# Kernel tuning notes

Hardware: AMD Instinct MI355X
Metric: run time of the kernel (lower is better)

## Reference

```python
import jax, jax.numpy as jnp
import numpy as np

N_NODES = 50000
N_EDGES = 1600000
DIM_IN = 128
DIM_OUT = 128
EPS = 1e-10


def setup_inputs() -> dict:
    key = jax.random.key(0)
    k1, k2, k3, k4, k5 = jax.random.split(key, 5)
    feat_in = jax.random.normal(k1, (N_NODES, DIM_IN), dtype=jnp.float32)
    rows = jax.random.randint(k2, (N_EDGES,), 0, N_NODES, dtype=jnp.int32)
    cols = jax.random.randint(k3, (N_EDGES,), 0, N_NODES, dtype=jnp.int32)
    # normalized adjacency values (positive, ~1/deg scale)
    vals = jax.random.uniform(k4, (N_EDGES,), dtype=jnp.float32) / 32.0
    W = jax.random.normal(k5, (DIM_OUT, DIM_IN), dtype=jnp.float32) * 0.05
    b = jnp.zeros((DIM_OUT,), dtype=jnp.float32)
    scale = jnp.ones((DIM_OUT,), dtype=jnp.float32)
    offset = jnp.zeros((DIM_OUT,), dtype=jnp.float32)
    return {"feat_in": feat_in, "rows": rows, "cols": cols, "vals": vals,
            "W": W, "b": b, "scale": scale, "offset": offset}


def reference(feat_in, rows, cols, vals, W, b, scale, offset):
    # torch.sparse.mm(adj_norm, feat_in): gather source features, scale by
    # edge value, scatter-add into destination rows.
    msgs = vals[:, None] * feat_in[cols]                       # [E, D_in]
    feat_aggr = jax.ops.segment_sum(msgs, rows, num_segments=N_NODES)  # [N, D_in]
    # f_lin (nn.Linear): x @ W.T + b
    feat_trans = feat_aggr @ W.T + b                           # [N, D_out]
    # act = ReLU
    a = jax.nn.relu(feat_trans)
    # f_norm: per-row (feature-dim) normalization, biased variance
    mean = jnp.mean(a, axis=1, keepdims=True)
    var = jnp.mean((a - mean) ** 2, axis=1, keepdims=True) + EPS
    feat_out = (a - mean) * scale * jax.lax.rsqrt(var) + offset
    return feat_out
```

## Files before the change

kernel.cpp:

```cpp
#include <hip/hip_runtime.h>

typedef unsigned int uint;
typedef unsigned short ushort;
typedef __attribute__((ext_vector_type(8))) short short8;
typedef __attribute__((ext_vector_type(4))) float floatx4;

#define N_NODES 50000
#define N_EDGES 1600000
#define DIM 128
#define LN_EPS 1e-10f

#define NB2 1564
#define CAP2 1280
#define EPB 6250
#define SB 256
#define CONVB 256
#define CAPR 76

__device__ __forceinline__ uint f2bf(float x) {
    uint u = __float_as_uint(x);
    return (u + 0x7FFFu + ((u >> 16) & 1u)) >> 16;
}

__global__ __launch_bounds__(1024, 8) void prep(
    const float* __restrict__ feat, const float* __restrict__ W,
    const int* __restrict__ rows, const int* __restrict__ cols,
    const float* __restrict__ vals, int* __restrict__ gcnt,
    int2* __restrict__ perm, uint* __restrict__ featb_u,
    ushort* __restrict__ wbf)
{
    __shared__ int  cnt[NB2];
    __shared__ int  gbase[NB2];
    __shared__ int  lbase[NB2];
    __shared__ int  csum[64];
    __shared__ int2 stageE[EPB];
    const int bx = blockIdx.x;
    const int t  = threadIdx.x;

    if (bx >= SB) {
        const int cb = bx - SB;
        const int stride = CONVB * 1024;
        for (int i = cb * 1024 + t; i < N_NODES * DIM / 4; i += stride) {
            float4 v = ((const float4*)feat)[i];
            ((uint2*)featb_u)[i] = make_uint2(
                f2bf(v.x) | (f2bf(v.y) << 16),
                f2bf(v.z) | (f2bf(v.w) << 16));
        }
        for (int i = cb * 1024 + t; i < DIM * DIM / 4; i += stride) {
            float4 v = ((const float4*)W)[i];
            ushort4 o;
            o.x = (ushort)f2bf(v.x); o.y = (ushort)f2bf(v.y);
            o.z = (ushort)f2bf(v.z); o.w = (ushort)f2bf(v.w);
            ((ushort4*)wbf)[i] = o;
        }
        return;
    }

    for (int i = t; i < NB2; i += 1024) cnt[i] = 0;
    __syncthreads();
    const int base = bx * EPB;
    uint pk[7];
    #pragma unroll
    for (int i = 0; i < 7; ++i) {
        int k = i * 1024 + t;
        if (k < EPB) {
            int r = rows[base + k];
            int rank = atomicAdd(&cnt[r >> 5], 1);
            pk[i] = ((uint)rank << 16) | (uint)r;
        }
    }
    __syncthreads();

    {
        const int rot = (bx * 16) % NB2;
        for (int i = t; i < NB2; i += 1024) {
            int ii = i + rot; if (ii >= NB2) ii -= NB2;
            int c = cnt[ii];
            gbase[ii] = c ? atomicAdd(&gcnt[ii], c) : 0;
        }
    }
    if (t < 64) {
        int s = 0;
        for (int j = 0; j < 25; ++j) {
            int idx = t * 25 + j;
            if (idx < NB2) s += cnt[idx];
        }
        csum[t] = s;
    }
    __syncthreads();
    if (t == 0) {
        int s = 0;
        for (int i = 0; i < 64; ++i) { int c = csum[i]; csum[i] = s; s += c; }
    }
    __syncthreads();
    if (t < 64) {
        int run = csum[t];
        for (int j = 0; j < 25; ++j) {
            int idx = t * 25 + j;
            if (idx < NB2) { lbase[idx] = run; run += cnt[idx]; }
        }
    }
    __syncthreads();

    #pragma unroll
    for (int i = 0; i < 7; ++i) {
        int k = i * 1024 + t;
        if (k < EPB) {
            uint s = pk[i];
            int r = (int)(s & 0xFFFFu);
            int rank = (int)(s >> 16);
            int b = r >> 5;
            int pos = lbase[b] + rank;
            stageE[pos] = make_int2(
                (uint)cols[base + k] | ((uint)(r & 31) << 16) | ((uint)b << 21),
                __float_as_int(vals[base + k]));
        }
    }
    __syncthreads();

    for (int j = t; j < EPB; j += 1024) {
        int2 p = stageE[j];
        uint b = ((uint)p.x) >> 21;
        int pos = gbase[b] + (j - lbase[b]);
        if (pos < CAP2)
            perm[(size_t)b * CAP2 + pos] = p;
    }
}

__global__ __launch_bounds__(512, 8) void agg_fused(
    const int2* __restrict__ perm, const int* __restrict__ gcnt,
    const ushort* __restrict__ featb, const ushort* __restrict__ wbf,
    const float* __restrict__ bias, const float* __restrict__ scale,
    const float* __restrict__ offset, float* __restrict__ out)
{
    __shared__ int2 lists[32 * CAPR];
    ushort* rowsbuf = (ushort*)lists;
    float*  Cbuf    = (float*)lists;
    __shared__ int  lcnt[32];

    const int t = threadIdx.x;

    const int q = NB2 >> 3, rr = NB2 & 7;
    const int xcd = blockIdx.x & 7, within = blockIdx.x >> 3;
    const int hb = (xcd < rr ? xcd * (q + 1) : rr * (q + 1) + (xcd - rr) * q) + within;

    if (t < 32) lcnt[t] = 0;
    __syncthreads();

    int n = gcnt[hb];
    if (n > CAP2) n = CAP2;
    const int2* pb = perm + (size_t)hb * CAP2;

    for (int e = t; e < n; e += 512) {
        int2 p = pb[e];
        int rl = (p.x >> 16) & 31;
        int pos = atomicAdd(&lcnt[rl], 1);
        if (pos < CAPR)
            lists[rl * CAPR + pos] = make_int2((p.x & 0xFFFF) << 8, p.y);
    }
    __syncthreads();

    const int lane = t & 63;
    const int wid  = t >> 6;
    const int rb   = wid * 4;
    const char* fbase = (const char*)featb;
    const uint  lane4 = (uint)lane << 2;

    float ax[4], ay[4];
    #pragma unroll
    for (int j = 0; j < 4; ++j) {
        int rl = rb + j;
        int cnt = lcnt[rl];
        if (cnt > CAPR) cnt = CAPR;
        const int2* L = &lists[rl * CAPR];
        float sx = 0.f, sy = 0.f;
        int e = 0;
        for (; e + 11 < cnt; e += 12) {
            int4 q6[6]; uint g[12];
            #pragma unroll
            for (int k = 0; k < 6; ++k) q6[k] = *(const int4*)&L[e + 2 * k];
            #pragma unroll
            for (int k = 0; k < 6; ++k) {
                g[2*k]   = *(const uint*)(fbase + ((uint)q6[k].x + lane4));
                g[2*k+1] = *(const uint*)(fbase + ((uint)q6[k].z + lane4));
            }
            #pragma unroll
            for (int k = 0; k < 6; ++k) {
                float v0 = __int_as_float(q6[k].y);
                float v1 = __int_as_float(q6[k].w);
                sx = fmaf(v0, __uint_as_float(g[2*k] << 16), sx);
                sy = fmaf(v0, __uint_as_float(g[2*k] & 0xFFFF0000u), sy);
                sx = fmaf(v1, __uint_as_float(g[2*k+1] << 16), sx);
                sy = fmaf(v1, __uint_as_float(g[2*k+1] & 0xFFFF0000u), sy);
            }
        }
        for (; e + 3 < cnt; e += 4) {
            int4 q2[2]; uint g[4];
            #pragma unroll
            for (int k = 0; k < 2; ++k) q2[k] = *(const int4*)&L[e + 2 * k];
            #pragma unroll
            for (int k = 0; k < 2; ++k) {
                g[2*k]   = *(const uint*)(fbase + ((uint)q2[k].x + lane4));
                g[2*k+1] = *(const uint*)(fbase + ((uint)q2[k].z + lane4));
            }
            #pragma unroll
            for (int k = 0; k < 2; ++k) {
                float v0 = __int_as_float(q2[k].y);
                float v1 = __int_as_float(q2[k].w);
                sx = fmaf(v0, __uint_as_float(g[2*k] << 16), sx);
                sy = fmaf(v0, __uint_as_float(g[2*k] & 0xFFFF0000u), sy);
                sx = fmaf(v1, __uint_as_float(g[2*k+1] << 16), sx);
                sy = fmaf(v1, __uint_as_float(g[2*k+1] & 0xFFFF0000u), sy);
            }
        }
        for (; e < cnt; ++e) {
            int2 p = L[e];
            uint g = *(const uint*)(fbase + ((uint)p.x + lane4));
            float v = __int_as_float(p.y);
            sx = fmaf(v, __uint_as_float(g << 16), sx);
            sy = fmaf(v, __uint_as_float(g & 0xFFFF0000u), sy);
        }
        ax[j] = sx; ay[j] = sy;
    }
    __syncthreads();

    #pragma unroll
    for (int j = 0; j < 4; ++j) {
        uint pk = f2bf(ax[j]) | (f2bf(ay[j]) << 16);
        *(uint*)&rowsbuf[(rb + j) * 136 + 2 * lane] = pk;
    }
    __syncthreads();

    const int l15  = lane & 15;
    const int quad = lane >> 4;
    const int n0   = wid * 16 + l15;
    const float bb = bias[n0];

    floatx4 acc0 = {0.f, 0.f, 0.f, 0.f};
    floatx4 acc1 = {0.f, 0.f, 0.f, 0.f};
    #pragma unroll
    for (int kt = 0; kt < 4; ++kt) {
        int k0 = kt * 32 + quad * 8;
        short8 af0 = *(const short8*)&rowsbuf[l15 * 136 + k0];
        short8 af1 = *(const short8*)&rowsbuf[(l15 + 16) * 136 + k0];
        short8 bf  = *(const short8*)&wbf[n0 * DIM + k0];
        acc0 = __builtin_amdgcn_mfma_f32_16x16x32_bf16(af0, bf, acc0, 0, 0, 0);
        acc1 = __builtin_amdgcn_mfma_f32_16x16x32_bf16(af1, bf, acc1, 0, 0, 0);
    }
    __syncthreads();

    #pragma unroll
    for (int r = 0; r < 4; ++r) {
        int m = quad * 4 + r;
        Cbuf[m * 132 + n0]        = acc0[r] + bb;
        Cbuf[(m + 16) * 132 + n0] = acc1[r] + bb;
    }
    __syncthreads();

    const float sc0 = scale[lane],  sc1 = scale[lane + 64];
    const float of0 = offset[lane], of1 = offset[lane + 64];

    #pragma unroll
    for (int j = 0; j < 4; ++j) {
        int rl = rb + j;
        int r  = hb * 32 + rl;
        if (r >= N_NODES) continue;
        float A0 = fmaxf(Cbuf[rl * 132 + lane],      0.0f);
        float A1 = fmaxf(Cbuf[rl * 132 + lane + 64], 0.0f);

        float s = A0 + A1;
        #pragma unroll
        for (int off = 32; off >= 1; off >>= 1) s += __shfl_xor(s, off, 64);
        float mean = s * (1.0f / 128.0f);

        float d0 = A0 - mean, d1 = A1 - mean;
        float q2 = d0 * d0 + d1 * d1;
        #pragma unroll
        for (int off = 32; off >= 1; off >>= 1) q2 += __shfl_xor(q2, off, 64);
        float rstd = rsqrtf(q2 * (1.0f / 128.0f) + LN_EPS);

        size_t rowp = (size_t)r * DIM;
        out[rowp + lane]      = d0 * sc0 * rstd + of0;
        out[rowp + lane + 64] = d1 * sc1 * rstd + of1;
    }
}

extern "C" void kernel_launch(void* const* d_in, const int* in_sizes, int n_in,
                              void* d_out, int out_size, void* d_ws, size_t ws_size,
                              hipStream_t stream) {
    const float* feat_in = (const float*)d_in[0];
    const int*   rows    = (const int*)d_in[1];
    const int*   cols    = (const int*)d_in[2];
    const float* vals    = (const float*)d_in[3];
    const float* W       = (const float*)d_in[4];
    const float* bias    = (const float*)d_in[5];
    const float* scale   = (const float*)d_in[6];
    const float* offset  = (const float*)d_in[7];
    float* out = (float*)d_out;

    char* p = (char*)d_ws;
    int2* perm = (int2*)p;                 p += (size_t)NB2 * CAP2 * 8;
    ushort* featb = (ushort*)p;            p += (size_t)N_NODES * DIM * 2;
    ushort* wbf = (ushort*)p;              p += DIM * DIM * 2;
    int*  gcnt = (int*)p;                  p += (size_t)(NB2 + 64) * 4;

    hipMemsetAsync(gcnt, 0, (size_t)NB2 * sizeof(int), stream);

    prep<<<SB + CONVB, 1024, 0, stream>>>(feat_in, W, rows, cols, vals,
                                          gcnt, perm, (uint*)featb, wbf);
    agg_fused<<<NB2, 512, 0, stream>>>(perm, gcnt, featb, wbf,
                                       bias, scale, offset, out);
}
```

Before: 170.7 us.

## Replace global atomic bucket reservation with histogram, scan and scatter passes

Splits the prep kernel into three kernels: a per-block histogram kernel that also does the bf16 conversion, a column-wise exclusive scan over the block histograms, and a scatter kernel that reads precomputed bases. This removes the per-bin global atomicAdd contention and the memset. It makes the bucket order deterministic, at the cost of two extra launches and a re-read of rows.

```diff
diff --git a/kernel.cpp b/kernel.cpp
--- a/kernel.cpp
+++ b/kernel.cpp
@@ -15,6 +15,7 @@
 #define EPB 6250
 #define SB 256
 #define CONVB 256
+#define TILES 49
 #define CAPR 76
 
 __device__ __forceinline__ uint f2bf(float x) {
@@ -22,12 +23,78 @@
     return (u + 0x7FFFu + ((u >> 16) & 1u)) >> 16;
 }
 
-__global__ __launch_bounds__(1024, 8) void prep(
+__global__ __launch_bounds__(1024) void hist_conv(
     const float* __restrict__ feat, const float* __restrict__ W,
+    const int* __restrict__ rows, int* __restrict__ histG,
+    uint* __restrict__ featb_u, ushort* __restrict__ wbf)
+{
+    __shared__ int cnt[NB2];
+    const int bx = blockIdx.x;
+    const int t  = threadIdx.x;
+
+    if (bx >= SB) {
+        const int cb = bx - SB;
+        const int stride = CONVB * 1024;
+        for (int i = cb * 1024 + t; i < N_NODES * DIM / 4; i += stride) {
+            float4 v = ((const float4*)feat)[i];
+            ((uint2*)featb_u)[i] = make_uint2(
+                f2bf(v.x) | (f2bf(v.y) << 16),
+                f2bf(v.z) | (f2bf(v.w) << 16));
+        }
+        for (int i = cb * 1024 + t; i < DIM * DIM / 4; i += stride) {
+            float4 v = ((const float4*)W)[i];
+            ushort4 o;
+            o.x = (ushort)f2bf(v.x); o.y = (ushort)f2bf(v.y);
+            o.z = (ushort)f2bf(v.z); o.w = (ushort)f2bf(v.w);
+            ((ushort4*)wbf)[i] = o;
+        }
+        return;
+    }
+
+    for (int i = t; i < NB2; i += 1024) cnt[i] = 0;
+    __syncthreads();
+    const int base = bx * EPB;
+    for (int k = t; k < EPB; k += 1024)
+        atomicAdd(&cnt[rows[base + k] >> 5], 1);
+    __syncthreads();
+    for (int i = t; i < NB2; i += 1024) histG[bx * NB2 + i] = cnt[i];
+}
+
+__global__ __launch_bounds__(1024) void scan(
+    const int* __restrict__ histG, int* __restrict__ baseG,
+    int* __restrict__ gcnt)
+{
+    __shared__ int tile[SB * 32];
+    const int bx = blockIdx.x;
+    const int t  = threadIdx.x;
+    const int t0 = bx * 32;
+
+    for (int i = t; i < SB * 32; i += 1024) {
+        int bin = t0 + (i & 31);
+        tile[i] = (bin < NB2) ? histG[(i >> 5) * NB2 + bin] : 0;
+    }
+    __syncthreads();
+    if (t < 32) {
+        int run = 0;
+        for (int r = 0; r < SB; ++r) {
+            int v = tile[r * 32 + t];
+            tile[r * 32 + t] = run;
+            run += v;
+        }
+        int bin = t0 + t;
+        if (bin < NB2) gcnt[bin] = run;
+    }
+    __syncthreads();
+    for (int i = t; i < SB * 32; i += 1024) {
+        int bin = t0 + (i & 31);
+        if (bin < NB2) baseG[(i >> 5) * NB2 + bin] = tile[i];
+    }
+}
+
+__global__ __launch_bounds__(1024, 8) void scatter3(
     const int* __restrict__ rows, const int* __restrict__ cols,
-    const float* __restrict__ vals, int* __restrict__ gcnt,
-    int2* __restrict__ perm, uint* __restrict__ featb_u,
-    ushort* __restrict__ wbf)
+    const float* __restrict__ vals, const int* __restrict__ baseG,
+    int2* __restrict__ perm)
 {
     __shared__ int  cnt[NB2];
     __shared__ int  gbase[NB2];
@@ -37,25 +104,6 @@
     const int bx = blockIdx.x;
     const int t  = threadIdx.x;
 
-    if (bx >= SB) {
-        const int cb = bx - SB;
-        const int stride = CONVB * 1024;
-        for (int i = cb * 1024 + t; i < N_NODES * DIM / 4; i += stride) {
-            float4 v = ((const float4*)feat)[i];
-            ((uint2*)featb_u)[i] = make_uint2(
-                f2bf(v.x) | (f2bf(v.y) << 16),
-                f2bf(v.z) | (f2bf(v.w) << 16));
-        }
-        for (int i = cb * 1024 + t; i < DIM * DIM / 4; i += stride) {
-            float4 v = ((const float4*)W)[i];
-            ushort4 o;
-            o.x = (ushort)f2bf(v.x); o.y = (ushort)f2bf(v.y);
-            o.z = (ushort)f2bf(v.z); o.w = (ushort)f2bf(v.w);
-            ((ushort4*)wbf)[i] = o;
-        }
-        return;
-    }
-
     for (int i = t; i < NB2; i += 1024) cnt[i] = 0;
     __syncthreads();
     const int base = bx * EPB;
@@ -71,14 +119,7 @@
     }
     __syncthreads();
 
-    {
-        const int rot = (bx * 16) % NB2;
-        for (int i = t; i < NB2; i += 1024) {
-            int ii = i + rot; if (ii >= NB2) ii -= NB2;
-            int c = cnt[ii];
-            gbase[ii] = c ? atomicAdd(&gcnt[ii], c) : 0;
-        }
-    }
+    for (int i = t; i < NB2; i += 1024) gbase[i] = baseG[bx * NB2 + i];
     if (t < 64) {
         int s = 0;
         for (int j = 0; j < 25; ++j) {
@@ -226,8 +267,8 @@
 
     #pragma unroll
     for (int j = 0; j < 4; ++j) {
-        uint pk = f2bf(ax[j]) | (f2bf(ay[j]) << 16);
-        *(uint*)&rowsbuf[(rb + j) * 136 + 2 * lane] = pk;
+        uint pkd = f2bf(ax[j]) | (f2bf(ay[j]) << 16);
+        *(uint*)&rowsbuf[(rb + j) * 136 + 2 * lane] = pkd;
     }
     __syncthreads();
 
@@ -303,11 +344,13 @@
     ushort* featb = (ushort*)p;            p += (size_t)N_NODES * DIM * 2;
     ushort* wbf = (ushort*)p;              p += DIM * DIM * 2;
     int*  gcnt = (int*)p;                  p += (size_t)(NB2 + 64) * 4;
-
-    hipMemsetAsync(gcnt, 0, (size_t)NB2 * sizeof(int), stream);
-
-    prep<<<SB + CONVB, 1024, 0, stream>>>(feat_in, W, rows, cols, vals,
-                                          gcnt, perm, (uint*)featb, wbf);
+    int*  histG = (int*)p;                 p += (size_t)SB * NB2 * 4;
+    int*  baseG = (int*)p;                 p += (size_t)SB * NB2 * 4;
+
+    hist_conv<<<SB + CONVB, 1024, 0, stream>>>(feat_in, W, rows, histG,
+                                               (uint*)featb, wbf);
+    scan<<<TILES, 1024, 0, stream>>>(histG, baseG, gcnt);
+    scatter3<<<SB, 1024, 0, stream>>>(rows, cols, vals, baseG, perm);
     agg_fused<<<NB2, 512, 0, stream>>>(perm, gcnt, featb, wbf,
                                        bias, scale, offset, out);
 }
```

Result: slower. 176.0 us (+3.1%).
